# Kernel optimization log

Hardware: AMD Instinct MI355X
Metric: run time of the kernel (lower is better)

## Reference

```python
import jax, jax.numpy as jnp
import numpy as np

STRIDES = [8, 16, 32, 64, 128]
FSIZES = [64, 32, 16, 8, 4]          # 512x512 input
NUM_CLASSES = 80
POS_THR, NEG_THR = 0.5, 0.4          # MaxIOUAssigner thresholds
BETA = 1.0 / 9.0                      # SmoothL1 beta (from loss_bbox cfg)
BBOX_W = 10.0                         # SmoothL1 loss_weight
ALPHA, GAMMA = 0.25, 2.0              # sigmoid focal loss


def _gen_anchors():
    """RetinaNet-style grid anchors, xyxy, concatenated over levels -> [A,4]."""
    ratios = np.array([0.5, 1.0, 2.0])
    scales = 4.0 * 2.0 ** (np.arange(3) / 3.0)   # octave_base_scale=4, 3 octaves
    levels = []
    for s, f in zip(STRIDES, FSIZES):
        ws = (s * scales[None, :] / np.sqrt(ratios)[:, None]).reshape(-1)  # [9]
        hs = (s * scales[None, :] * np.sqrt(ratios)[:, None]).reshape(-1)
        c = (np.arange(f) + 0.5) * s
        sx, sy = np.meshgrid(c, c)
        cxy = np.stack([sx, sy], -1).reshape(-1, 1, 2)   # [f*f,1,2]
        wh = np.stack([ws, hs], -1)[None]                # [1,9,2]
        a = np.concatenate([cxy - wh / 2, cxy + wh / 2], -1).reshape(-1, 4)
        levels.append(a)
    return jnp.asarray(np.concatenate(levels, 0), dtype=jnp.float32)  # [49104,4]


def _iou(anchors, gt):  # [A,4],[M,4] -> [A,M]
    area_a = (anchors[:, 2] - anchors[:, 0]) * (anchors[:, 3] - anchors[:, 1])
    area_g = (gt[:, 2] - gt[:, 0]) * (gt[:, 3] - gt[:, 1])
    lt = jnp.maximum(anchors[:, None, :2], gt[None, :, :2])
    rb = jnp.minimum(anchors[:, None, 2:], gt[None, :, 2:])
    wh = jnp.clip(rb - lt, 0.0)
    inter = wh[..., 0] * wh[..., 1]
    return inter / jnp.maximum(area_a[:, None] + area_g[None, :] - inter, 1e-6)


def _encode(boxes, anchors):  # DeltaXYWH encode, target_stds = 1
    aw = anchors[:, 2] - anchors[:, 0]
    ah = anchors[:, 3] - anchors[:, 1]
    ax = (anchors[:, 0] + anchors[:, 2]) * 0.5
    ay = (anchors[:, 1] + anchors[:, 3]) * 0.5
    gw = jnp.maximum(boxes[:, 2] - boxes[:, 0], 1e-6)
    gh = jnp.maximum(boxes[:, 3] - boxes[:, 1], 1e-6)
    gx = (boxes[:, 0] + boxes[:, 2]) * 0.5
    gy = (boxes[:, 1] + boxes[:, 3]) * 0.5
    return jnp.stack([(gx - ax) / aw, (gy - ay) / ah,
                      jnp.log(gw / aw), jnp.log(gh / ah)], -1)


def _assign_one(gt_boxes, gt_labels, gt_mask, anchors):
    """Per-image: IoU match, pseudo-sample, gather matched GT, encode, masks."""
    iou = _iou(anchors, gt_boxes)                      # [A,M]
    iou = jnp.where(gt_mask[None, :], iou, -1.0)       # kill padded GTs
    best = jnp.argmax(iou, 1)                          # [A]
    best_iou = jnp.max(iou, 1)
    # matched index: >=0 matched, -1 background, -2 ignored
    idx = jnp.where(best_iou >= POS_THR, best,
                    jnp.where(best_iou < NEG_THR, -1, -2))
    pos = idx >= 0
    matched = jnp.where(pos[:, None], gt_boxes[best], 0.0)   # gather_based_on_match
    reg_t = _encode(matched, anchors)
    total = jnp.maximum(1.0, jnp.sum(pos.astype(jnp.float32)))
    mask_reg = pos.astype(jnp.float32)[:, None] / total      # [A,1] -> broadcast 4
    labels = jnp.where(pos, gt_labels[best], -1)             # bg/ignored -> -1
    mask_cls = (idx >= -1).astype(jnp.float32) / total       # matched + background
    return reg_t, mask_reg, labels, mask_cls


def setup_inputs() -> dict:
    key = jax.random.key(0)
    ks = jax.random.split(key, 6)
    B, M, A, C = 16, 100, 49104, NUM_CLASSES
    cls_score = jax.random.normal(ks[0], (B, A, C), jnp.float32)
    bbox_pred = jax.random.normal(ks[1], (B, A, 4), jnp.float32) * 0.1
    cxy = jax.random.uniform(ks[2], (B, M, 2), jnp.float32, 50.0, 462.0)
    wh = jax.random.uniform(ks[3], (B, M, 2), jnp.float32, 16.0, 128.0)
    target_boxes = jnp.concatenate([cxy - wh / 2, cxy + wh / 2], -1)
    target_labels = jax.random.randint(ks[4], (B, M), 0, C, jnp.int32)
    mask_labels = jax.random.randint(ks[5], (B, M), 0, 2, jnp.int32).astype(bool)
    return {"cls_score": cls_score, "bbox_pred": bbox_pred,
            "target_boxes": target_boxes, "target_labels": target_labels,
            "mask_labels": mask_labels}


def reference(cls_score, bbox_pred, target_boxes, target_labels, mask_labels):
    anchors = _gen_anchors()                                        # [A,4]
    reg_t, mask_reg, labels, mask_cls = jax.vmap(
        _assign_one, in_axes=(0, 0, 0, None))(
        target_boxes, target_labels, mask_labels, anchors)          # per image
    bs = float(cls_score.shape[0])
    # SmoothL1 (beta=1/9, weight 10), masked + normalized per image
    d = jnp.abs(bbox_pred - reg_t)
    l1 = jnp.where(d < BETA, 0.5 * d * d / BETA, d - 0.5 * BETA)
    loss_bbox = BBOX_W * jnp.sum(l1 * mask_reg) / bs
    # sigmoid focal loss
    t = jax.nn.one_hot(labels, NUM_CLASSES, dtype=cls_score.dtype)  # -1 -> all-zero
    bce = t * jax.nn.softplus(-cls_score) + (1.0 - t) * jax.nn.softplus(cls_score)
    p = jax.nn.sigmoid(cls_score)
    pt = t * p + (1.0 - t) * (1.0 - p)
    at = ALPHA * t + (1.0 - ALPHA) * (1.0 - t)
    focal = at * (1.0 - pt) ** GAMMA * bce
    loss_cls = jnp.sum(focal * mask_cls[..., None]) / bs
    return jnp.stack([loss_cls, loss_bbox])
```

## Files before the change

kernel.cpp:

```cpp
#include <hip/hip_runtime.h>

#define N_ANCH 49104
#define NB_IMG 16
#define NGT 100
#define NC 80
#define BPI 96
#define APB 512
#define NBLK (BPI * NB_IMG)
#define OFF_B NBLK
#define OFF_P (2 * NBLK)

#define LOG2E 1.4426950408889634f
#define LN2   0.6931471805599453f
#define FSCALE (0.75f * LN2)

__device__ __forceinline__ float frcp(float x){ return __builtin_amdgcn_rcpf(x); }
__device__ __forceinline__ float fexp2(float x){ return __builtin_amdgcn_exp2f(x); }
__device__ __forceinline__ float flog2(float x){ return __builtin_amdgcn_logf(x); }

__device__ __forceinline__ float f0_term(float x){
  float xl = x * LOG2E;
  float mx = fmaxf(xl, 0.f);
  float mn = fminf(xl, 0.f);
  float u  = fexp2(mn - mx);
  float w  = 1.0f + u;
  float lw = flog2(w);
  float g  = mn - lw;
  return fexp2(g + g) * (lw + mx);
}

__device__ __forceinline__ float corr_term(float x){
  float xl = x * LOG2E;
  float mx = fmaxf(xl, 0.f);
  float mn = fminf(xl, 0.f);
  float u  = fexp2(mn - mx);
  float w  = 1.0f + u;
  float lw = flog2(w);
  float p2   = fexp2(2.f * (mn - lw));
  float omp2 = fexp2(-2.f * (mx + lw));
  float sp   = LN2 * (lw + mx);
  float spn  = LN2 * (lw - mn);
  return 0.25f * omp2 * spn - 0.75f * p2 * sp;
}

__global__ __launch_bounds__(256, 6) void fused_loss_kernel(
    const float* __restrict__ cls,
    const float* __restrict__ bbox,
    const float* __restrict__ gtb,
    const int*   __restrict__ gtl,
    const unsigned char* __restrict__ gmask,
    float* __restrict__ ws)
{
  const int tid = threadIdx.x;
  const int wv = tid >> 6, ln = tid & 63;
  const int b  = blockIdx.y;
  const int a0 = blockIdx.x * APB;
  const int bid = b * BPI + blockIdx.x;

  __shared__ float4 s_cgt[NGT + 4];
  __shared__ float  s_carea[NGT + 4];
  __shared__ int    s_clab[NGT + 4];
  __shared__ float  s_w[APB];
  __shared__ int    s_lab[APB];
  __shared__ float  s_wmin[4], s_wmax[4];
  __shared__ float  s_r0[4], s_r1[4], s_r2[4];
  __shared__ int    s_cnt;

  float ax1[2], ay1[2], ax2[2], ay2[2], aarea[2];
  #pragma unroll
  for (int r = 0; r < 2; ++r){
    int a = a0 + r * 256 + tid;
    if (a < N_ANCH){
      int f, lg, st, rel;
      if      (a < 36864){ f = 64; lg = 6; st = 8;   rel = a; }
      else if (a < 46080){ f = 32; lg = 5; st = 16;  rel = a - 36864; }
      else if (a < 48384){ f = 16; lg = 4; st = 32;  rel = a - 46080; }
      else if (a < 48960){ f = 8;  lg = 3; st = 64;  rel = a - 48384; }
      else               { f = 4;  lg = 2; st = 128; rel = a - 48960; }
      int cell = rel / 9;
      int k    = rel - cell * 9;
      int yy   = cell >> lg;
      int xx   = cell & (f - 1);
      int rr = (k >= 6) ? 2 : ((k >= 3) ? 1 : 0);
      int sc = k - rr * 3;
      double sq  = (rr == 0) ? 0.7071067811865476 : ((rr == 1) ? 1.0 : 1.4142135623730951);
      double scl = (sc == 0) ? 4.0 : ((sc == 1) ? 5.039684199579493 : 6.349604207872798);
      double ss  = (double)st * scl;
      double wd  = ss / sq, hd = ss * sq;
      double cxd = ((double)xx + 0.5) * (double)st;
      double cyd = ((double)yy + 0.5) * (double)st;
      ax1[r] = (float)(cxd - wd * 0.5);
      ay1[r] = (float)(cyd - hd * 0.5);
      ax2[r] = (float)(cxd + wd * 0.5);
      ay2[r] = (float)(cyd + hd * 0.5);
      aarea[r] = (ax2[r] - ax1[r]) * (ay2[r] - ay1[r]);
    } else {
      ax1[r] = 0.f; ay1[r] = 3.0e38f; ax2[r] = 0.f; ay2[r] = -3.0e38f; aarea[r] = 1.f;
    }
  }

  {
    float wy1 = fminf(ay1[0], ay1[1]);
    float wy2 = fmaxf(ay2[0], ay2[1]);
    #pragma unroll
    for (int o = 32; o > 0; o >>= 1){
      wy1 = fminf(wy1, __shfl_down(wy1, o));
      wy2 = fmaxf(wy2, __shfl_down(wy2, o));
    }
    if (ln == 0){ s_wmin[wv] = wy1; s_wmax[wv] = wy2; }
  }
  __syncthreads();

  if (wv == 0){
    const unsigned int* mw = (const unsigned int*)gmask;
    bool nf = false, ob = false;
    for (int i = ln; i < (NB_IMG * NGT) / 4; i += 64){
      unsigned int w = mw[i];
      nf |= (w != 0u && w != 0x3F800000u);
      ob |= ((w & 0xFFFFFF00u) != 0u);
    }
    bool byteLayout = __any((int)nf) && __any((int)ob);
    float ymin = fminf(fminf(s_wmin[0], s_wmin[1]), fminf(s_wmin[2], s_wmin[3]));
    float ymax = fmaxf(fmaxf(s_wmax[0], s_wmax[1]), fmaxf(s_wmax[2], s_wmax[3]));
    const float4* g4 = (const float4*)gtb;

    float4 g = g4[b * NGT + ln];
    int v = byteLayout ? (gmask[b * NGT + ln] != 0)
                       : (((const unsigned int*)gmask)[b * NGT + ln] != 0u);
    bool pass = v && (g.y < ymax) && (g.w > ymin);
    unsigned long long bal = __ballot(pass);
    int pre = __popcll(bal & ((1ull << ln) - 1ull));
    if (pass){
      s_cgt[pre] = g;
      s_carea[pre] = (g.z - g.x) * (g.w - g.y);
      s_clab[pre] = gtl[b * NGT + ln];
    }
    int c0 = __popcll(bal);
    bool pass1 = false; float4 g1;
    if (ln < NGT - 64){
      g1 = g4[b * NGT + 64 + ln];
      int v1 = byteLayout ? (gmask[b * NGT + 64 + ln] != 0)
                          : (((const unsigned int*)gmask)[b * NGT + 64 + ln] != 0u);
      pass1 = v1 && (g1.y < ymax) && (g1.w > ymin);
    }
    unsigned long long bal1 = __ballot(pass1);
    int pre1 = c0 + __popcll(bal1 & ((1ull << ln) - 1ull));
    if (pass1){
      s_cgt[pre1] = g1;
      s_carea[pre1] = (g1.z - g1.x) * (g1.w - g1.y);
      s_clab[pre1] = gtl[b * NGT + 64 + ln];
    }
    if (ln == 0){
      int cnt = c0 + __popcll(bal1);
      float4 far4; far4.x = 3e9f; far4.y = 3e9f; far4.z = 3e9f; far4.w = 3e9f;
      s_cgt[cnt] = far4;     s_carea[cnt] = 0.f;     s_clab[cnt] = 0;
      s_cgt[cnt + 1] = far4; s_carea[cnt + 1] = 0.f; s_clab[cnt + 1] = 0;
      s_cnt = (cnt + 1) & ~1;
    }
  }
  __syncthreads();

  float accB = 0.f, posf = 0.f, fcorr = 0.f;
  const int cntp = s_cnt;
  #pragma unroll
  for (int r = 0; r < 2; ++r){
    int row = r * 256 + tid;
    int a = a0 + row;
    float x1 = ax1[r], y1 = ay1[r], x2 = ax2[r], y2 = ay2[r], areaA = aarea[r];
    float best_iou = -1.f; int best = 0;
    for (int j = 0; j < cntp; j += 2){
      #pragma unroll
      for (int u2 = 0; u2 < 2; ++u2){
        int jj = j + u2;
        float4 g = s_cgt[jj];
        float lx = fmaxf(x1, g.x), ly = fmaxf(y1, g.y);
        float rx = fminf(x2, g.z), ry = fminf(y2, g.w);
        float iw = fmaxf(rx - lx, 0.f), ih = fmaxf(ry - ly, 0.f);
        float I  = iw * ih;
        float U  = (areaA + s_carea[jj]) - I;
        float iou = I * frcp(U);
        best = (iou > best_iou) ? jj : best;
        best_iou = fmaxf(iou, best_iou);
      }
    }
    bool va  = a < N_ANCH;
    bool pos = va && (best_iou >= 0.5f);
    bool ign = va && !pos && (best_iou >= 0.4f);
    s_w[row]   = (va && !ign) ? 1.f : 0.f;
    s_lab[row] = pos ? s_clab[best] : -1;

    if (pos){
      posf += 1.f;
      float4 g = s_cgt[best];
      float aw = x2 - x1, ah = y2 - y1;
      float axc = (x1 + x2) * 0.5f, ayc = (y1 + y2) * 0.5f;
      float gw = fmaxf(g.z - g.x, 1e-6f), gh = fmaxf(g.w - g.y, 1e-6f);
      float gxc = (g.x + g.z) * 0.5f, gyc = (g.y + g.w) * 0.5f;
      float t0 = (gxc - axc) / aw, t1 = (gyc - ayc) / ah;
      float t2 = LN2 * flog2(gw * frcp(aw));
      float t3 = LN2 * flog2(gh * frcp(ah));
      float4 bp = ((const float4*)bbox)[(size_t)b * N_ANCH + a];
      const float BETA = 1.0f / 9.0f;
      float d0 = fabsf(bp.x - t0), d1 = fabsf(bp.y - t1);
      float d2 = fabsf(bp.z - t2), d3 = fabsf(bp.w - t3);
      accB += (d0 < BETA) ? 4.5f * d0 * d0 : d0 - 0.5f * BETA;
      accB += (d1 < BETA) ? 4.5f * d1 * d1 : d1 - 0.5f * BETA;
      accB += (d2 < BETA) ? 4.5f * d2 * d2 : d2 - 0.5f * BETA;
      accB += (d3 < BETA) ? 4.5f * d3 * d3 : d3 - 0.5f * BETA;
    }
  }
  __syncthreads();

  const int nvalid = min(N_ANCH - a0, APB);
  const int nf4 = nvalid * 20;
  const float4* cp = (const float4*)(cls + (size_t)(b * N_ANCH + a0) * NC);
  float fraw = 0.f;
  for (int i = tid; i < nf4; i += 256){
    float4 c4 = cp[i];
    int row = i / 20;
    int cb  = (i - row * 20) * 4;
    float s = (f0_term(c4.x) + f0_term(c4.y)) + (f0_term(c4.z) + f0_term(c4.w));
    fraw = fmaf(s_w[row], s, fraw);
    int lab = s_lab[row];
    if ((unsigned)(lab - cb) < 4u){
      int o = lab - cb;
      float xe = (o == 0) ? c4.x : (o == 1) ? c4.y : (o == 2) ? c4.z : c4.w;
      fcorr += corr_term(xe);
    }
  }
  float accC = fmaf(FSCALE, fraw, fcorr);

  #pragma unroll
  for (int o = 32; o > 0; o >>= 1){
    accC += __shfl_down(accC, o);
    accB += __shfl_down(accB, o);
    posf += __shfl_down(posf, o);
  }
  if (ln == 0){ s_r0[wv] = accC; s_r1[wv] = accB; s_r2[wv] = posf; }
  __syncthreads();
  if (tid == 0){
    ws[bid]         = s_r0[0] + s_r0[1] + s_r0[2] + s_r0[3];
    ws[OFF_B + bid] = s_r1[0] + s_r1[1] + s_r1[2] + s_r1[3];
    ws[OFF_P + bid] = s_r2[0] + s_r2[1] + s_r2[2] + s_r2[3];
  }
}

__global__ void finalize_kernel(const float* __restrict__ ws,
                                float* __restrict__ out)
{
  __shared__ float sC[NB_IMG], sB[NB_IMG];
  const int tid = threadIdx.x;
  const int wv = tid >> 6, ln = tid & 63;
  #pragma unroll
  for (int i = 0; i < 2; ++i){
    int b = wv * 2 + i;
    float c = 0.f, bb = 0.f, p = 0.f;
    for (int k = ln; k < BPI; k += 64){
      c  += ws[b * BPI + k];
      bb += ws[OFF_B + b * BPI + k];
      p  += ws[OFF_P + b * BPI + k];
    }
    #pragma unroll
    for (int o = 32; o > 0; o >>= 1){
      c += __shfl_down(c, o); bb += __shfl_down(bb, o); p += __shfl_down(p, o);
    }
    if (ln == 0){
      float tot = fmaxf(p, 1.f);
      sC[b] = c / tot;
      sB[b] = bb / tot;
    }
  }
  __syncthreads();
  if (tid == 0){
    float lc = 0.f, lb = 0.f;
    #pragma unroll
    for (int b = 0; b < NB_IMG; ++b){ lc += sC[b]; lb += sB[b]; }
    out[0] = lc / 16.f;
    out[1] = 10.f * lb / 16.f;
  }
}

extern "C" void kernel_launch(void* const* d_in, const int* in_sizes, int n_in,
                              void* d_out, int out_size, void* d_ws, size_t ws_size,
                              hipStream_t stream) {
  const float* cls  = (const float*)d_in[0];
  const float* bbox = (const float*)d_in[1];
  const float* gtb  = (const float*)d_in[2];
  const int*   gtl  = (const int*)d_in[3];
  const unsigned char* gmask = (const unsigned char*)d_in[4];

  float* ws = (float*)d_ws;

  dim3 grid(BPI, NB_IMG);
  fused_loss_kernel<<<grid, 256, 0, stream>>>(cls, bbox, gtb, gtl, gmask, ws);
  finalize_kernel<<<1, 512, 0, stream>>>(ws, (float*)d_out);
}
```

Baseline: 57.25 us.

## Overlap anchor assignment in one wave with unweighted focal streaming

Wave 3 of each block now does all the anchor generation, GT compaction and IoU matching for the block's 512 anchors. Meanwhile all four waves stream the class scores and sum the focal negative term without weights. Rows marked ignored are then re-read and their contribution subtracted, and the positive-label correction reads one element per row directly. This removes the barrier between assignment and the bandwidth-heavy class-score pass. In exchange, the IoU work sits on a single wave, which may lengthen that wave's critical path, and ignored rows are read twice.

```diff
diff --git a/kernel.cpp b/kernel.cpp
--- a/kernel.cpp
+++ b/kernel.cpp
@@ -9,6 +9,9 @@
 #define NBLK (BPI * NB_IMG)
 #define OFF_B NBLK
 #define OFF_P (2 * NBLK)
+#define ROW_F4 (NC / 4)
+#define BLK_F4 (APB * ROW_F4)
+#define WCHUNK (BLK_F4 / 4)
 
 #define LOG2E 1.4426950408889634f
 #define LN2   0.6931471805599453f
@@ -41,6 +44,32 @@
   float sp   = LN2 * (lw + mx);
   float spn  = LN2 * (lw - mn);
   return 0.25f * omp2 * spn - 0.75f * p2 * sp;
+}
+
+__device__ __forceinline__ void anchor_geom(int a, float& x1, float& y1,
+                                            float& x2, float& y2){
+  int f, lg, st, rel;
+  if      (a < 36864){ f = 64; lg = 6; st = 8;   rel = a; }
+  else if (a < 46080){ f = 32; lg = 5; st = 16;  rel = a - 36864; }
+  else if (a < 48384){ f = 16; lg = 4; st = 32;  rel = a - 46080; }
+  else if (a < 48960){ f = 8;  lg = 3; st = 64;  rel = a - 48384; }
+  else               { f = 4;  lg = 2; st = 128; rel = a - 48960; }
+  int cell = rel / 9;
+  int k    = rel - cell * 9;
+  int yy   = cell >> lg;
+  int xx   = cell & (f - 1);
+  int rr = (k >= 6) ? 2 : ((k >= 3) ? 1 : 0);
+  int sc = k - rr * 3;
+  double sq  = (rr == 0) ? 0.7071067811865476 : ((rr == 1) ? 1.0 : 1.4142135623730951);
+  double scl = (sc == 0) ? 4.0 : ((sc == 1) ? 5.039684199579493 : 6.349604207872798);
+  double ss  = (double)st * scl;
+  double wd  = ss / sq, hd = ss * sq;
+  double cxd = ((double)xx + 0.5) * (double)st;
+  double cyd = ((double)yy + 0.5) * (double)st;
+  x1 = (float)(cxd - wd * 0.5);
+  y1 = (float)(cyd - hd * 0.5);
+  x2 = (float)(cxd + wd * 0.5);
+  y2 = (float)(cyd + hd * 0.5);
 }
 
 __global__ __launch_bounds__(256, 6) void fused_loss_kernel(
@@ -56,62 +85,40 @@
   const int b  = blockIdx.y;
   const int a0 = blockIdx.x * APB;
   const int bid = b * BPI + blockIdx.x;
+  const int nvalid = min(N_ANCH - a0, APB);
+  const int nf4 = nvalid * ROW_F4;
 
   __shared__ float4 s_cgt[NGT + 4];
   __shared__ float  s_carea[NGT + 4];
   __shared__ int    s_clab[NGT + 4];
   __shared__ float  s_w[APB];
   __shared__ int    s_lab[APB];
-  __shared__ float  s_wmin[4], s_wmax[4];
   __shared__ float  s_r0[4], s_r1[4], s_r2[4];
-  __shared__ int    s_cnt;
-
-  float ax1[2], ay1[2], ax2[2], ay2[2], aarea[2];
-  #pragma unroll
-  for (int r = 0; r < 2; ++r){
-    int a = a0 + r * 256 + tid;
-    if (a < N_ANCH){
-      int f, lg, st, rel;
-      if      (a < 36864){ f = 64; lg = 6; st = 8;   rel = a; }
-      else if (a < 46080){ f = 32; lg = 5; st = 16;  rel = a - 36864; }
-      else if (a < 48384){ f = 16; lg = 4; st = 32;  rel = a - 46080; }
-      else if (a < 48960){ f = 8;  lg = 3; st = 64;  rel = a - 48384; }
-      else               { f = 4;  lg = 2; st = 128; rel = a - 48960; }
-      int cell = rel / 9;
-      int k    = rel - cell * 9;
-      int yy   = cell >> lg;
-      int xx   = cell & (f - 1);
-      int rr = (k >= 6) ? 2 : ((k >= 3) ? 1 : 0);
-      int sc = k - rr * 3;
-      double sq  = (rr == 0) ? 0.7071067811865476 : ((rr == 1) ? 1.0 : 1.4142135623730951);
-      double scl = (sc == 0) ? 4.0 : ((sc == 1) ? 5.039684199579493 : 6.349604207872798);
-      double ss  = (double)st * scl;
-      double wd  = ss / sq, hd = ss * sq;
-      double cxd = ((double)xx + 0.5) * (double)st;
-      double cyd = ((double)yy + 0.5) * (double)st;
-      ax1[r] = (float)(cxd - wd * 0.5);
-      ay1[r] = (float)(cyd - hd * 0.5);
-      ax2[r] = (float)(cxd + wd * 0.5);
-      ay2[r] = (float)(cyd + hd * 0.5);
-      aarea[r] = (ax2[r] - ax1[r]) * (ay2[r] - ay1[r]);
-    } else {
-      ax1[r] = 0.f; ay1[r] = 3.0e38f; ax2[r] = 0.f; ay2[r] = -3.0e38f; aarea[r] = 1.f;
-    }
-  }
-
-  {
-    float wy1 = fminf(ay1[0], ay1[1]);
-    float wy2 = fmaxf(ay2[0], ay2[1]);
+
+  const float* clsbase = cls + (size_t)(b * N_ANCH + a0) * NC;
+  const float4* cp = (const float4*)clsbase;
+
+  float accB = 0.f, posf = 0.f;
+  float s0 = 0.f, s1 = 0.f, s2 = 0.f, s3 = 0.f;
+
+  if (wv == 3){
+    float ymin = 3.0e38f, ymax = -3.0e38f;
     #pragma unroll
-    for (int o = 32; o > 0; o >>= 1){
-      wy1 = fminf(wy1, __shfl_down(wy1, o));
-      wy2 = fmaxf(wy2, __shfl_down(wy2, o));
-    }
-    if (ln == 0){ s_wmin[wv] = wy1; s_wmax[wv] = wy2; }
-  }
-  __syncthreads();
-
-  if (wv == 0){
+    for (int r = 0; r < 8; ++r){
+      int a = a0 + r * 64 + ln;
+      if (a < N_ANCH){
+        float x1, y1, x2, y2;
+        anchor_geom(a, x1, y1, x2, y2);
+        ymin = fminf(ymin, y1);
+        ymax = fmaxf(ymax, y2);
+      }
+    }
+    #pragma unroll
+    for (int o = 1; o < 64; o <<= 1){
+      ymin = fminf(ymin, __shfl_xor(ymin, o));
+      ymax = fmaxf(ymax, __shfl_xor(ymax, o));
+    }
+
     const unsigned int* mw = (const unsigned int*)gmask;
     bool nf = false, ob = false;
     for (int i = ln; i < (NB_IMG * NGT) / 4; i += 64){
@@ -120,10 +127,8 @@
       ob |= ((w & 0xFFFFFF00u) != 0u);
     }
     bool byteLayout = __any((int)nf) && __any((int)ob);
-    float ymin = fminf(fminf(s_wmin[0], s_wmin[1]), fminf(s_wmin[2], s_wmin[3]));
-    float ymax = fmaxf(fmaxf(s_wmax[0], s_wmax[1]), fmaxf(s_wmax[2], s_wmax[3]));
+
     const float4* g4 = (const float4*)gtb;
-
     float4 g = g4[b * NGT + ln];
     int v = byteLayout ? (gmask[b * NGT + ln] != 0)
                        : (((const unsigned int*)gmask)[b * NGT + ln] != 0u);
@@ -150,85 +155,99 @@
       s_carea[pre1] = (g1.z - g1.x) * (g1.w - g1.y);
       s_clab[pre1] = gtl[b * NGT + 64 + ln];
     }
+    int cnt = c0 + __popcll(bal1);
     if (ln == 0){
-      int cnt = c0 + __popcll(bal1);
       float4 far4; far4.x = 3e9f; far4.y = 3e9f; far4.z = 3e9f; far4.w = 3e9f;
       s_cgt[cnt] = far4;     s_carea[cnt] = 0.f;     s_clab[cnt] = 0;
       s_cgt[cnt + 1] = far4; s_carea[cnt + 1] = 0.f; s_clab[cnt + 1] = 0;
-      s_cnt = (cnt + 1) & ~1;
+    }
+    const int cntp = (cnt + 1) & ~1;
+
+    #pragma unroll 2
+    for (int r = 0; r < 8; ++r){
+      int row = r * 64 + ln;
+      int a = a0 + row;
+      float x1, y1, x2, y2;
+      anchor_geom(min(a, N_ANCH - 1), x1, y1, x2, y2);
+      float areaA = (x2 - x1) * (y2 - y1);
+      float best_iou = -1.f; int best = 0;
+      for (int j = 0; j < cntp; j += 2){
+        #pragma unroll
+        for (int u2 = 0; u2 < 2; ++u2){
+          int jj = j + u2;
+          float4 gg = s_cgt[jj];
+          float lx = fmaxf(x1, gg.x), ly = fmaxf(y1, gg.y);
+          float rx = fminf(x2, gg.z), ry = fminf(y2, gg.w);
+          float iw = fmaxf(rx - lx, 0.f), ih = fmaxf(ry - ly, 0.f);
+          float I  = iw * ih;
+          float U  = (areaA + s_carea[jj]) - I;
+          float iou = I * frcp(U);
+          best = (iou > best_iou) ? jj : best;
+          best_iou = fmaxf(iou, best_iou);
+        }
+      }
+      bool va  = a < N_ANCH;
+      bool pos = va && (best_iou >= 0.5f);
+      bool ign = va && !pos && (best_iou >= 0.4f);
+      s_w[row]   = ign ? 0.f : 1.f;
+      s_lab[row] = pos ? s_clab[best] : -1;
+
+      if (pos){
+        posf += 1.f;
+        float4 gg = s_cgt[best];
+        float aw = x2 - x1, ah = y2 - y1;
+        float axc = (x1 + x2) * 0.5f, ayc = (y1 + y2) * 0.5f;
+        float gw = fmaxf(gg.z - gg.x, 1e-6f), gh = fmaxf(gg.w - gg.y, 1e-6f);
+        float gxc = (gg.x + gg.z) * 0.5f, gyc = (gg.y + gg.w) * 0.5f;
+        float t0 = (gxc - axc) / aw, t1 = (gyc - ayc) / ah;
+        float t2 = LN2 * flog2(gw * frcp(aw));
+        float t3 = LN2 * flog2(gh * frcp(ah));
+        float4 bp = ((const float4*)bbox)[(size_t)b * N_ANCH + a];
+        const float BETA = 1.0f / 9.0f;
+        float d0 = fabsf(bp.x - t0), d1 = fabsf(bp.y - t1);
+        float d2 = fabsf(bp.z - t2), d3 = fabsf(bp.w - t3);
+        accB += (d0 < BETA) ? 4.5f * d0 * d0 : d0 - 0.5f * BETA;
+        accB += (d1 < BETA) ? 4.5f * d1 * d1 : d1 - 0.5f * BETA;
+        accB += (d2 < BETA) ? 4.5f * d2 * d2 : d2 - 0.5f * BETA;
+        accB += (d3 < BETA) ? 4.5f * d3 * d3 : d3 - 0.5f * BETA;
+      }
+    }
+  }
+
+  {
+    const int iend = min(nf4, (wv + 1) * WCHUNK);
+    #pragma unroll 2
+    for (int i = wv * WCHUNK + ln; i < iend; i += 64){
+      float4 c4 = cp[i];
+      s0 += f0_term(c4.x);
+      s1 += f0_term(c4.y);
+      s2 += f0_term(c4.z);
+      s3 += f0_term(c4.w);
     }
   }
   __syncthreads();
 
-  float accB = 0.f, posf = 0.f, fcorr = 0.f;
-  const int cntp = s_cnt;
+  float fsub = 0.f, fcorr = 0.f;
   #pragma unroll
-  for (int r = 0; r < 2; ++r){
-    int row = r * 256 + tid;
-    int a = a0 + row;
-    float x1 = ax1[r], y1 = ay1[r], x2 = ax2[r], y2 = ay2[r], areaA = aarea[r];
-    float best_iou = -1.f; int best = 0;
-    for (int j = 0; j < cntp; j += 2){
-      #pragma unroll
-      for (int u2 = 0; u2 < 2; ++u2){
-        int jj = j + u2;
-        float4 g = s_cgt[jj];
-        float lx = fmaxf(x1, g.x), ly = fmaxf(y1, g.y);
-        float rx = fminf(x2, g.z), ry = fminf(y2, g.w);
-        float iw = fmaxf(rx - lx, 0.f), ih = fmaxf(ry - ly, 0.f);
-        float I  = iw * ih;
-        float U  = (areaA + s_carea[jj]) - I;
-        float iou = I * frcp(U);
-        best = (iou > best_iou) ? jj : best;
-        best_iou = fmaxf(iou, best_iou);
+  for (int h = 0; h < 2; ++h){
+    int row = wv * 128 + h * 64 + ln;
+    if (row < nvalid){
+      int lab = s_lab[row];
+      if (lab >= 0) fcorr += corr_term(clsbase[row * NC + lab]);
+      if (s_w[row] == 0.f){
+        const float4* rp = cp + row * ROW_F4;
+        float t0 = 0.f, t1 = 0.f, t2 = 0.f, t3 = 0.f;
+        #pragma unroll 5
+        for (int k2 = 0; k2 < ROW_F4; ++k2){
+          float4 c4 = rp[k2];
+          t0 += f0_term(c4.x); t1 += f0_term(c4.y);
+          t2 += f0_term(c4.z); t3 += f0_term(c4.w);
+        }
+        fsub += (t0 + t1) + (t2 + t3);
       }
     }
-    bool va  = a < N_ANCH;
-    bool pos = va && (best_iou >= 0.5f);
-    bool ign = va && !pos && (best_iou >= 0.4f);
-    s_w[row]   = (va && !ign) ? 1.f : 0.f;
-    s_lab[row] = pos ? s_clab[best] : -1;
-
-    if (pos){
-      posf += 1.f;
-      float4 g = s_cgt[best];
-      float aw = x2 - x1, ah = y2 - y1;
-      float axc = (x1 + x2) * 0.5f, ayc = (y1 + y2) * 0.5f;
-      float gw = fmaxf(g.z - g.x, 1e-6f), gh = fmaxf(g.w - g.y, 1e-6f);
-      float gxc = (g.x + g.z) * 0.5f, gyc = (g.y + g.w) * 0.5f;
-      float t0 = (gxc - axc) / aw, t1 = (gyc - ayc) / ah;
-      float t2 = LN2 * flog2(gw * frcp(aw));
-      float t3 = LN2 * flog2(gh * frcp(ah));
-      float4 bp = ((const float4*)bbox)[(size_t)b * N_ANCH + a];
-      const float BETA = 1.0f / 9.0f;
-      float d0 = fabsf(bp.x - t0), d1 = fabsf(bp.y - t1);
-      float d2 = fabsf(bp.z - t2), d3 = fabsf(bp.w - t3);
-      accB += (d0 < BETA) ? 4.5f * d0 * d0 : d0 - 0.5f * BETA;
-      accB += (d1 < BETA) ? 4.5f * d1 * d1 : d1 - 0.5f * BETA;
-      accB += (d2 < BETA) ? 4.5f * d2 * d2 : d2 - 0.5f * BETA;
-      accB += (d3 < BETA) ? 4.5f * d3 * d3 : d3 - 0.5f * BETA;
-    }
-  }
-  __syncthreads();
-
-  const int nvalid = min(N_ANCH - a0, APB);
-  const int nf4 = nvalid * 20;
-  const float4* cp = (const float4*)(cls + (size_t)(b * N_ANCH + a0) * NC);
-  float fraw = 0.f;
-  for (int i = tid; i < nf4; i += 256){
-    float4 c4 = cp[i];
-    int row = i / 20;
-    int cb  = (i - row * 20) * 4;
-    float s = (f0_term(c4.x) + f0_term(c4.y)) + (f0_term(c4.z) + f0_term(c4.w));
-    fraw = fmaf(s_w[row], s, fraw);
-    int lab = s_lab[row];
-    if ((unsigned)(lab - cb) < 4u){
-      int o = lab - cb;
-      float xe = (o == 0) ? c4.x : (o == 1) ? c4.y : (o == 2) ? c4.z : c4.w;
-      fcorr += corr_term(xe);
-    }
-  }
-  float accC = fmaf(FSCALE, fraw, fcorr);
+  }
+  float accC = fmaf(FSCALE, ((s0 + s1) + (s2 + s3)) - fsub, fcorr);
 
   #pragma unroll
   for (int o = 32; o > 0; o >>= 1){
```

New measurement: 89.50 us. 1.56x slower.

## Split fused loss into separate assign and cls-streaming kernels with byte label buffer

Applied to the files above, without the earlier changes.

Splits the single fused kernel into an IoU-assignment kernel, which writes per-anchor byte labels (with neg/ignore sentinels) plus the bbox partial sums, and a separate streaming kernel that reads the labels and computes focal loss over cls_score. The IoU argmax now compares by cross-multiplication instead of taking a reciprocal, and thresholds are tested the same way. The intent is to keep the bandwidth-bound cls stream free of the compute-heavy assignment phase and its syncs. In exchange it adds a kernel launch and a global round trip for the label buffer.

```diff
diff --git a/kernel.cpp b/kernel.cpp
--- a/kernel.cpp
+++ b/kernel.cpp
@@ -7,12 +7,15 @@
 #define BPI 96
 #define APB 512
 #define NBLK (BPI * NB_IMG)
-#define OFF_B NBLK
-#define OFF_P (2 * NBLK)
+#define ROW_F4 (NC / 4)
+#define LABSTRIDE (BPI * APB)
 
 #define LOG2E 1.4426950408889634f
 #define LN2   0.6931471805599453f
 #define FSCALE (0.75f * LN2)
+
+#define LAB_NEG 200
+#define LAB_IGN 201
 
 __device__ __forceinline__ float frcp(float x){ return __builtin_amdgcn_rcpf(x); }
 __device__ __forceinline__ float fexp2(float x){ return __builtin_amdgcn_exp2f(x); }
@@ -43,62 +46,65 @@
   return 0.25f * omp2 * spn - 0.75f * p2 * sp;
 }
 
-__global__ __launch_bounds__(256, 6) void fused_loss_kernel(
-    const float* __restrict__ cls,
+__device__ __forceinline__ void anchor_geom(int a, float& x1, float& y1,
+                                            float& x2, float& y2){
+  int lg, st, rel;
+  if      (a < 36864){ lg = 6; st = 8;   rel = a; }
+  else if (a < 46080){ lg = 5; st = 16;  rel = a - 36864; }
+  else if (a < 48384){ lg = 4; st = 32;  rel = a - 46080; }
+  else if (a < 48960){ lg = 3; st = 64;  rel = a - 48384; }
+  else               { lg = 2; st = 128; rel = a - 48960; }
+  int cell = rel / 9;
+  int k    = rel - cell * 9;
+  int yy   = cell >> lg;
+  int xx   = cell & ((1 << lg) - 1);
+  int rr = (k >= 6) ? 2 : ((k >= 3) ? 1 : 0);
+  int sc = k - rr * 3;
+  double sq  = (rr == 0) ? 0.7071067811865476 : ((rr == 1) ? 1.0 : 1.4142135623730951);
+  double scl = (sc == 0) ? 4.0 : ((sc == 1) ? 5.039684199579493 : 6.349604207872798);
+  double ss  = (double)st * scl;
+  double wd  = ss / sq, hd = ss * sq;
+  double cxd = ((double)xx + 0.5) * (double)st;
+  double cyd = ((double)yy + 0.5) * (double)st;
+  x1 = (float)(cxd - wd * 0.5);
+  y1 = (float)(cyd - hd * 0.5);
+  x2 = (float)(cxd + wd * 0.5);
+  y2 = (float)(cyd + hd * 0.5);
+}
+
+__global__ __launch_bounds__(256, 6) void assign_kernel(
     const float* __restrict__ bbox,
     const float* __restrict__ gtb,
     const int*   __restrict__ gtl,
     const unsigned char* __restrict__ gmask,
-    float* __restrict__ ws)
+    unsigned char* __restrict__ lab,
+    float* __restrict__ bbP,
+    float* __restrict__ posP)
 {
   const int tid = threadIdx.x;
   const int wv = tid >> 6, ln = tid & 63;
   const int b  = blockIdx.y;
-  const int a0 = blockIdx.x * APB;
-  const int bid = b * BPI + blockIdx.x;
+  const int blkx = blockIdx.x;
+  const int a0 = blkx * APB;
+  const int bid = b * BPI + blkx;
 
   __shared__ float4 s_cgt[NGT + 4];
   __shared__ float  s_carea[NGT + 4];
   __shared__ int    s_clab[NGT + 4];
-  __shared__ float  s_w[APB];
-  __shared__ int    s_lab[APB];
   __shared__ float  s_wmin[4], s_wmax[4];
-  __shared__ float  s_r0[4], s_r1[4], s_r2[4];
+  __shared__ float  s_r1[4], s_r2[4];
   __shared__ int    s_cnt;
 
-  float ax1[2], ay1[2], ax2[2], ay2[2], aarea[2];
+  float ax1[2], ay1[2], ax2[2], ay2[2];
   #pragma unroll
   for (int r = 0; r < 2; ++r){
     int a = a0 + r * 256 + tid;
     if (a < N_ANCH){
-      int f, lg, st, rel;
-      if      (a < 36864){ f = 64; lg = 6; st = 8;   rel = a; }
-      else if (a < 46080){ f = 32; lg = 5; st = 16;  rel = a - 36864; }
-      else if (a < 48384){ f = 16; lg = 4; st = 32;  rel = a - 46080; }
-      else if (a < 48960){ f = 8;  lg = 3; st = 64;  rel = a - 48384; }
-      else               { f = 4;  lg = 2; st = 128; rel = a - 48960; }
-      int cell = rel / 9;
-      int k    = rel - cell * 9;
-      int yy   = cell >> lg;
-      int xx   = cell & (f - 1);
-      int rr = (k >= 6) ? 2 : ((k >= 3) ? 1 : 0);
-      int sc = k - rr * 3;
-      double sq  = (rr == 0) ? 0.7071067811865476 : ((rr == 1) ? 1.0 : 1.4142135623730951);
-      double scl = (sc == 0) ? 4.0 : ((sc == 1) ? 5.039684199579493 : 6.349604207872798);
-      double ss  = (double)st * scl;
-      double wd  = ss / sq, hd = ss * sq;
-      double cxd = ((double)xx + 0.5) * (double)st;
-      double cyd = ((double)yy + 0.5) * (double)st;
-      ax1[r] = (float)(cxd - wd * 0.5);
-      ay1[r] = (float)(cyd - hd * 0.5);
-      ax2[r] = (float)(cxd + wd * 0.5);
-      ay2[r] = (float)(cyd + hd * 0.5);
-      aarea[r] = (ax2[r] - ax1[r]) * (ay2[r] - ay1[r]);
+      anchor_geom(a, ax1[r], ay1[r], ax2[r], ay2[r]);
     } else {
-      ax1[r] = 0.f; ay1[r] = 3.0e38f; ax2[r] = 0.f; ay2[r] = -3.0e38f; aarea[r] = 1.f;
-    }
-  }
-
+      ax1[r] = 0.f; ay1[r] = 3.0e38f; ax2[r] = 0.f; ay2[r] = -3.0e38f;
+    }
+  }
   {
     float wy1 = fminf(ay1[0], ay1[1]);
     float wy2 = fmaxf(ay2[0], ay2[1]);
@@ -160,42 +166,45 @@
   }
   __syncthreads();
 
-  float accB = 0.f, posf = 0.f, fcorr = 0.f;
+  float accB = 0.f, posf = 0.f;
   const int cntp = s_cnt;
   #pragma unroll
   for (int r = 0; r < 2; ++r){
-    int row = r * 256 + tid;
-    int a = a0 + row;
-    float x1 = ax1[r], y1 = ay1[r], x2 = ax2[r], y2 = ay2[r], areaA = aarea[r];
-    float best_iou = -1.f; int best = 0;
+    int a = a0 + r * 256 + tid;
+    float x1 = ax1[r], y1 = ay1[r], x2 = ax2[r], y2 = ay2[r];
+    float areaA = (x2 - x1) * (y2 - y1);
+    float Ib = -1.f, Ub = 1.f; int best = 0;
     for (int j = 0; j < cntp; j += 2){
       #pragma unroll
       for (int u2 = 0; u2 < 2; ++u2){
         int jj = j + u2;
-        float4 g = s_cgt[jj];
-        float lx = fmaxf(x1, g.x), ly = fmaxf(y1, g.y);
-        float rx = fminf(x2, g.z), ry = fminf(y2, g.w);
+        float4 gg = s_cgt[jj];
+        float lx = fmaxf(x1, gg.x), ly = fmaxf(y1, gg.y);
+        float rx = fminf(x2, gg.z), ry = fminf(y2, gg.w);
         float iw = fmaxf(rx - lx, 0.f), ih = fmaxf(ry - ly, 0.f);
         float I  = iw * ih;
         float U  = (areaA + s_carea[jj]) - I;
-        float iou = I * frcp(U);
-        best = (iou > best_iou) ? jj : best;
-        best_iou = fmaxf(iou, best_iou);
+        bool gt = I * Ub > Ib * U;
+        best = gt ? jj : best;
+        Ib = gt ? I : Ib;
+        Ub = gt ? U : Ub;
       }
     }
     bool va  = a < N_ANCH;
-    bool pos = va && (best_iou >= 0.5f);
-    bool ign = va && !pos && (best_iou >= 0.4f);
-    s_w[row]   = (va && !ign) ? 1.f : 0.f;
-    s_lab[row] = pos ? s_clab[best] : -1;
+    bool pos = va && (2.f * Ib >= Ub);
+    bool ign = !pos && (5.f * Ib >= 2.f * Ub);
+    unsigned char lb = pos ? (unsigned char)s_clab[best]
+                           : ((ign || !va) ? (unsigned char)LAB_IGN
+                                           : (unsigned char)LAB_NEG);
+    lab[(size_t)b * LABSTRIDE + a0 + r * 256 + tid] = lb;
 
     if (pos){
       posf += 1.f;
-      float4 g = s_cgt[best];
+      float4 gg = s_cgt[best];
       float aw = x2 - x1, ah = y2 - y1;
       float axc = (x1 + x2) * 0.5f, ayc = (y1 + y2) * 0.5f;
-      float gw = fmaxf(g.z - g.x, 1e-6f), gh = fmaxf(g.w - g.y, 1e-6f);
-      float gxc = (g.x + g.z) * 0.5f, gyc = (g.y + g.w) * 0.5f;
+      float gw = fmaxf(gg.z - gg.x, 1e-6f), gh = fmaxf(gg.w - gg.y, 1e-6f);
+      float gxc = (gg.x + gg.z) * 0.5f, gyc = (gg.y + gg.w) * 0.5f;
       float t0 = (gxc - axc) / aw, t1 = (gyc - ayc) / ah;
       float t2 = LN2 * flog2(gw * frcp(aw));
       float t3 = LN2 * flog2(gh * frcp(ah));
@@ -209,21 +218,53 @@
       accB += (d3 < BETA) ? 4.5f * d3 * d3 : d3 - 0.5f * BETA;
     }
   }
-  __syncthreads();
-
+
+  #pragma unroll
+  for (int o = 32; o > 0; o >>= 1){
+    accB += __shfl_down(accB, o);
+    posf += __shfl_down(posf, o);
+  }
+  if (ln == 0){ s_r1[wv] = accB; s_r2[wv] = posf; }
+  __syncthreads();
+  if (tid == 0){
+    bbP[bid]  = s_r1[0] + s_r1[1] + s_r1[2] + s_r1[3];
+    posP[bid] = s_r2[0] + s_r2[1] + s_r2[2] + s_r2[3];
+  }
+}
+
+__global__ __launch_bounds__(256, 6) void stream_kernel(
+    const float* __restrict__ cls,
+    const unsigned char* __restrict__ lab,
+    float* __restrict__ clsP)
+{
+  const int tid = threadIdx.x;
+  const int wv = tid >> 6, ln = tid & 63;
+  const int b  = blockIdx.y;
+  const int a0 = blockIdx.x * APB;
+  const int bid = b * BPI + blockIdx.x;
   const int nvalid = min(N_ANCH - a0, APB);
-  const int nf4 = nvalid * 20;
+  const int nf4 = nvalid * ROW_F4;
+
+  __shared__ unsigned char s_lab[APB];
+  __shared__ float s_r0[4];
+
+  #pragma unroll
+  for (int j = 0; j < 2; ++j)
+    s_lab[j * 256 + tid] = lab[(size_t)b * LABSTRIDE + a0 + j * 256 + tid];
+  __syncthreads();
+
   const float4* cp = (const float4*)(cls + (size_t)(b * N_ANCH + a0) * NC);
-  float fraw = 0.f;
+  float fraw = 0.f, fcorr = 0.f;
   for (int i = tid; i < nf4; i += 256){
     float4 c4 = cp[i];
     int row = i / 20;
     int cb  = (i - row * 20) * 4;
     float s = (f0_term(c4.x) + f0_term(c4.y)) + (f0_term(c4.z) + f0_term(c4.w));
-    fraw = fmaf(s_w[row], s, fraw);
-    int lab = s_lab[row];
-    if ((unsigned)(lab - cb) < 4u){
-      int o = lab - cb;
+    int li = (int)s_lab[row];
+    float wf = (li == LAB_IGN) ? 0.f : 1.f;
+    fraw = fmaf(wf, s, fraw);
+    if ((unsigned)(li - cb) < 4u){
+      int o = li - cb;
       float xe = (o == 0) ? c4.x : (o == 1) ? c4.y : (o == 2) ? c4.z : c4.w;
       fcorr += corr_term(xe);
     }
@@ -231,21 +272,15 @@
   float accC = fmaf(FSCALE, fraw, fcorr);
 
   #pragma unroll
-  for (int o = 32; o > 0; o >>= 1){
-    accC += __shfl_down(accC, o);
-    accB += __shfl_down(accB, o);
-    posf += __shfl_down(posf, o);
-  }
-  if (ln == 0){ s_r0[wv] = accC; s_r1[wv] = accB; s_r2[wv] = posf; }
-  __syncthreads();
-  if (tid == 0){
-    ws[bid]         = s_r0[0] + s_r0[1] + s_r0[2] + s_r0[3];
-    ws[OFF_B + bid] = s_r1[0] + s_r1[1] + s_r1[2] + s_r1[3];
-    ws[OFF_P + bid] = s_r2[0] + s_r2[1] + s_r2[2] + s_r2[3];
-  }
-}
-
-__global__ void finalize_kernel(const float* __restrict__ ws,
+  for (int o = 32; o > 0; o >>= 1) accC += __shfl_down(accC, o);
+  if (ln == 0) s_r0[wv] = accC;
+  __syncthreads();
+  if (tid == 0) clsP[bid] = s_r0[0] + s_r0[1] + s_r0[2] + s_r0[3];
+}
+
+__global__ void finalize_kernel(const float* __restrict__ clsP,
+                                const float* __restrict__ bbP,
+                                const float* __restrict__ posP,
                                 float* __restrict__ out)
 {
   __shared__ float sC[NB_IMG], sB[NB_IMG];
@@ -256,9 +291,9 @@
     int b = wv * 2 + i;
     float c = 0.f, bb = 0.f, p = 0.f;
     for (int k = ln; k < BPI; k += 64){
-      c  += ws[b * BPI + k];
-      bb += ws[OFF_B + b * BPI + k];
-      p  += ws[OFF_P + b * BPI + k];
+      c  += clsP[b * BPI + k];
+      bb += bbP[b * BPI + k];
+      p  += posP[b * BPI + k];
     }
     #pragma unroll
     for (int o = 32; o > 0; o >>= 1){
@@ -289,9 +324,14 @@
   const int*   gtl  = (const int*)d_in[3];
   const unsigned char* gmask = (const unsigned char*)d_in[4];
 
-  float* ws = (float*)d_ws;
+  unsigned char* labbuf = (unsigned char*)d_ws;
+  float* wsf  = (float*)((char*)d_ws + (size_t)NB_IMG * LABSTRIDE);
+  float* bbP  = wsf;
+  float* posP = wsf + NBLK;
+  float* clsP = wsf + 2 * NBLK;
 
   dim3 grid(BPI, NB_IMG);
-  fused_loss_kernel<<<grid, 256, 0, stream>>>(cls, bbox, gtb, gtl, gmask, ws);
-  finalize_kernel<<<1, 512, 0, stream>>>(ws, (float*)d_out);
-}
+  assign_kernel<<<grid, 256, 0, stream>>>(bbox, gtb, gtl, gmask, labbuf, bbP, posP);
+  stream_kernel<<<grid, 256, 0, stream>>>(cls, labbuf, clsP);
+  finalize_kernel<<<1, 512, 0, stream>>>(clsP, bbP, posP, (float*)d_out);
+}
```

New measurement: 66.14 us. +15.5%, slower.

## Per-wave GT compaction, divide-free IoU compare, prefetch cls, direct label correction

Applied to the files above, without the earlier changes.

Each wave now builds its own compacted GT list in shared memory using a wave-wide ymin/ymax reduction, which removes two block barriers and the wave-0 serialization. Anchor geometry moves from double precision to float arithmetic with constant tables. IoU argmax compares I*U cross products instead of computing reciprocals, and the thresholds are tested the same way. The focal label correction is read directly for positive anchors, which drops the per-element label check from the streaming loop, and the first two cls float4 loads are issued at kernel start to overlap with matching. The risks are that every wave redundantly scans the mask and GT data, and that float anchor coordinates or the cross-product comparison could differ slightly from the reference at threshold and tie boundaries.

```diff
diff --git a/kernel.cpp b/kernel.cpp
--- a/kernel.cpp
+++ b/kernel.cpp
@@ -7,12 +7,35 @@
 #define BPI 96
 #define APB 512
 #define NBLK (BPI * NB_IMG)
-#define OFF_B NBLK
-#define OFF_P (2 * NBLK)
+#define ROW_F4 (NC / 4)
+#define MAXG 104
 
 #define LOG2E 1.4426950408889634f
 #define LN2   0.6931471805599453f
 #define FSCALE (0.75f * LN2)
+
+__constant__ float BW9[9] = {
+  (float)(4.0               / 0.7071067811865476 * 0.5),
+  (float)(5.039684199579493 / 0.7071067811865476 * 0.5),
+  (float)(6.349604207872798 / 0.7071067811865476 * 0.5),
+  (float)(4.0               * 0.5),
+  (float)(5.039684199579493 * 0.5),
+  (float)(6.349604207872798 * 0.5),
+  (float)(4.0               / 1.4142135623730951 * 0.5),
+  (float)(5.039684199579493 / 1.4142135623730951 * 0.5),
+  (float)(6.349604207872798 / 1.4142135623730951 * 0.5),
+};
+__constant__ float BH9[9] = {
+  (float)(4.0               * 0.7071067811865476 * 0.5),
+  (float)(5.039684199579493 * 0.7071067811865476 * 0.5),
+  (float)(6.349604207872798 * 0.7071067811865476 * 0.5),
+  (float)(4.0               * 0.5),
+  (float)(5.039684199579493 * 0.5),
+  (float)(6.349604207872798 * 0.5),
+  (float)(4.0               * 1.4142135623730951 * 0.5),
+  (float)(5.039684199579493 * 1.4142135623730951 * 0.5),
+  (float)(6.349604207872798 * 1.4142135623730951 * 0.5),
+};
 
 __device__ __forceinline__ float frcp(float x){ return __builtin_amdgcn_rcpf(x); }
 __device__ __forceinline__ float fexp2(float x){ return __builtin_amdgcn_exp2f(x); }
@@ -27,6 +50,9 @@
   float lw = flog2(w);
   float g  = mn - lw;
   return fexp2(g + g) * (lw + mx);
+}
+__device__ __forceinline__ float f0x4(float4 c4){
+  return (f0_term(c4.x) + f0_term(c4.y)) + (f0_term(c4.z) + f0_term(c4.w));
 }
 
 __device__ __forceinline__ float corr_term(float x){
@@ -41,6 +67,26 @@
   float sp   = LN2 * (lw + mx);
   float spn  = LN2 * (lw - mn);
   return 0.25f * omp2 * spn - 0.75f * p2 * sp;
+}
+
+__device__ __forceinline__ void anchor_geom(int a, float& x1, float& y1,
+                                            float& x2, float& y2){
+  int lg, st, rel;
+  if      (a < 36864){ lg = 6; st = 8;   rel = a; }
+  else if (a < 46080){ lg = 5; st = 16;  rel = a - 36864; }
+  else if (a < 48384){ lg = 4; st = 32;  rel = a - 46080; }
+  else if (a < 48960){ lg = 3; st = 64;  rel = a - 48384; }
+  else               { lg = 2; st = 128; rel = a - 48960; }
+  int cell = rel / 9;
+  int k    = rel - cell * 9;
+  int yy   = cell >> lg;
+  int xx   = cell & ((1 << lg) - 1);
+  float stf = (float)st;
+  float cx = ((float)xx + 0.5f) * stf;
+  float cy = ((float)yy + 0.5f) * stf;
+  float w2 = stf * BW9[k];
+  float h2 = stf * BH9[k];
+  x1 = cx - w2; y1 = cy - h2; x2 = cx + w2; y2 = cy + h2;
 }
 
 __global__ __launch_bounds__(256, 6) void fused_loss_kernel(
@@ -56,146 +102,117 @@
   const int b  = blockIdx.y;
   const int a0 = blockIdx.x * APB;
   const int bid = b * BPI + blockIdx.x;
-
-  __shared__ float4 s_cgt[NGT + 4];
-  __shared__ float  s_carea[NGT + 4];
-  __shared__ int    s_clab[NGT + 4];
-  __shared__ float  s_w[APB];
-  __shared__ int    s_lab[APB];
-  __shared__ float  s_wmin[4], s_wmax[4];
+  const int nvalid = min(N_ANCH - a0, APB);
+  const int nf4 = nvalid * ROW_F4;
+
+  __shared__ float4 s_cgt[4][MAXG];
+  __shared__ float  s_carea[4][MAXG];
+  __shared__ int    s_clab[4][MAXG];
+  __shared__ float  s_wf[APB];
   __shared__ float  s_r0[4], s_r1[4], s_r2[4];
-  __shared__ int    s_cnt;
-
-  float ax1[2], ay1[2], ax2[2], ay2[2], aarea[2];
+
+  const float* clsbase = cls + (size_t)(b * N_ANCH + a0) * NC;
+  const float4* cp = (const float4*)clsbase;
+
+  float4 pf0 = cp[tid];
+  float4 pf1 = cp[tid + 256];
+
+  float ax1[2], ay1[2], ax2[2], ay2[2];
   #pragma unroll
   for (int r = 0; r < 2; ++r){
     int a = a0 + r * 256 + tid;
-    if (a < N_ANCH){
-      int f, lg, st, rel;
-      if      (a < 36864){ f = 64; lg = 6; st = 8;   rel = a; }
-      else if (a < 46080){ f = 32; lg = 5; st = 16;  rel = a - 36864; }
-      else if (a < 48384){ f = 16; lg = 4; st = 32;  rel = a - 46080; }
-      else if (a < 48960){ f = 8;  lg = 3; st = 64;  rel = a - 48384; }
-      else               { f = 4;  lg = 2; st = 128; rel = a - 48960; }
-      int cell = rel / 9;
-      int k    = rel - cell * 9;
-      int yy   = cell >> lg;
-      int xx   = cell & (f - 1);
-      int rr = (k >= 6) ? 2 : ((k >= 3) ? 1 : 0);
-      int sc = k - rr * 3;
-      double sq  = (rr == 0) ? 0.7071067811865476 : ((rr == 1) ? 1.0 : 1.4142135623730951);
-      double scl = (sc == 0) ? 4.0 : ((sc == 1) ? 5.039684199579493 : 6.349604207872798);
-      double ss  = (double)st * scl;
-      double wd  = ss / sq, hd = ss * sq;
-      double cxd = ((double)xx + 0.5) * (double)st;
-      double cyd = ((double)yy + 0.5) * (double)st;
-      ax1[r] = (float)(cxd - wd * 0.5);
-      ay1[r] = (float)(cyd - hd * 0.5);
-      ax2[r] = (float)(cxd + wd * 0.5);
-      ay2[r] = (float)(cyd + hd * 0.5);
-      aarea[r] = (ax2[r] - ax1[r]) * (ay2[r] - ay1[r]);
-    } else {
-      ax1[r] = 0.f; ay1[r] = 3.0e38f; ax2[r] = 0.f; ay2[r] = -3.0e38f; aarea[r] = 1.f;
-    }
-  }
-
-  {
-    float wy1 = fminf(ay1[0], ay1[1]);
-    float wy2 = fmaxf(ay2[0], ay2[1]);
-    #pragma unroll
-    for (int o = 32; o > 0; o >>= 1){
-      wy1 = fminf(wy1, __shfl_down(wy1, o));
-      wy2 = fmaxf(wy2, __shfl_down(wy2, o));
-    }
-    if (ln == 0){ s_wmin[wv] = wy1; s_wmax[wv] = wy2; }
-  }
-  __syncthreads();
-
-  if (wv == 0){
-    const unsigned int* mw = (const unsigned int*)gmask;
-    bool nf = false, ob = false;
-    for (int i = ln; i < (NB_IMG * NGT) / 4; i += 64){
-      unsigned int w = mw[i];
-      nf |= (w != 0u && w != 0x3F800000u);
-      ob |= ((w & 0xFFFFFF00u) != 0u);
-    }
-    bool byteLayout = __any((int)nf) && __any((int)ob);
-    float ymin = fminf(fminf(s_wmin[0], s_wmin[1]), fminf(s_wmin[2], s_wmin[3]));
-    float ymax = fmaxf(fmaxf(s_wmax[0], s_wmax[1]), fmaxf(s_wmax[2], s_wmax[3]));
-    const float4* g4 = (const float4*)gtb;
-
-    float4 g = g4[b * NGT + ln];
-    int v = byteLayout ? (gmask[b * NGT + ln] != 0)
-                       : (((const unsigned int*)gmask)[b * NGT + ln] != 0u);
-    bool pass = v && (g.y < ymax) && (g.w > ymin);
-    unsigned long long bal = __ballot(pass);
-    int pre = __popcll(bal & ((1ull << ln) - 1ull));
-    if (pass){
-      s_cgt[pre] = g;
-      s_carea[pre] = (g.z - g.x) * (g.w - g.y);
-      s_clab[pre] = gtl[b * NGT + ln];
-    }
-    int c0 = __popcll(bal);
-    bool pass1 = false; float4 g1;
-    if (ln < NGT - 64){
-      g1 = g4[b * NGT + 64 + ln];
-      int v1 = byteLayout ? (gmask[b * NGT + 64 + ln] != 0)
-                          : (((const unsigned int*)gmask)[b * NGT + 64 + ln] != 0u);
-      pass1 = v1 && (g1.y < ymax) && (g1.w > ymin);
-    }
-    unsigned long long bal1 = __ballot(pass1);
-    int pre1 = c0 + __popcll(bal1 & ((1ull << ln) - 1ull));
-    if (pass1){
-      s_cgt[pre1] = g1;
-      s_carea[pre1] = (g1.z - g1.x) * (g1.w - g1.y);
-      s_clab[pre1] = gtl[b * NGT + 64 + ln];
-    }
-    if (ln == 0){
-      int cnt = c0 + __popcll(bal1);
-      float4 far4; far4.x = 3e9f; far4.y = 3e9f; far4.z = 3e9f; far4.w = 3e9f;
-      s_cgt[cnt] = far4;     s_carea[cnt] = 0.f;     s_clab[cnt] = 0;
-      s_cgt[cnt + 1] = far4; s_carea[cnt + 1] = 0.f; s_clab[cnt + 1] = 0;
-      s_cnt = (cnt + 1) & ~1;
-    }
-  }
-  __syncthreads();
+    if (a < N_ANCH) anchor_geom(a, ax1[r], ay1[r], ax2[r], ay2[r]);
+    else { ax1[r] = 0.f; ay1[r] = 3.0e38f; ax2[r] = 0.f; ay2[r] = -3.0e38f; }
+  }
+
+  float ymin = fminf(ay1[0], ay1[1]);
+  float ymax = fmaxf(ay2[0], ay2[1]);
+  #pragma unroll
+  for (int o = 32; o > 0; o >>= 1){
+    ymin = fminf(ymin, __shfl_xor(ymin, o));
+    ymax = fmaxf(ymax, __shfl_xor(ymax, o));
+  }
+
+  const unsigned int* mw = (const unsigned int*)gmask;
+  bool nfb = false, ob = false;
+  for (int i = ln; i < (NB_IMG * NGT) / 4; i += 64){
+    unsigned int w = mw[i];
+    nfb |= (w != 0u && w != 0x3F800000u);
+    ob  |= ((w & 0xFFFFFF00u) != 0u);
+  }
+  const bool byteLayout = __any((int)nfb) && __any((int)ob);
+
+  const float4* g4 = (const float4*)gtb;
+  float4 g = g4[b * NGT + ln];
+  int v = byteLayout ? (gmask[b * NGT + ln] != 0)
+                     : (((const unsigned int*)gmask)[b * NGT + ln] != 0u);
+  bool pass = v && (g.y < ymax) && (g.w > ymin);
+  unsigned long long bal = __ballot(pass);
+  int pre = __popcll(bal & ((1ull << ln) - 1ull));
+  if (pass){
+    s_cgt[wv][pre]   = g;
+    s_carea[wv][pre] = (g.z - g.x) * (g.w - g.y);
+    s_clab[wv][pre]  = gtl[b * NGT + ln];
+  }
+  int cnt = __popcll(bal);
+  float4 g1; bool pass1 = false;
+  if (ln < NGT - 64){
+    g1 = g4[b * NGT + 64 + ln];
+    int v1 = byteLayout ? (gmask[b * NGT + 64 + ln] != 0)
+                        : (((const unsigned int*)gmask)[b * NGT + 64 + ln] != 0u);
+    pass1 = v1 && (g1.y < ymax) && (g1.w > ymin);
+  }
+  unsigned long long bal1 = __ballot(pass1);
+  int pre1 = cnt + __popcll(bal1 & ((1ull << ln) - 1ull));
+  if (pass1){
+    s_cgt[wv][pre1]   = g1;
+    s_carea[wv][pre1] = (g1.z - g1.x) * (g1.w - g1.y);
+    s_clab[wv][pre1]  = gtl[b * NGT + 64 + ln];
+  }
+  cnt += __popcll(bal1);
+  if (ln == 0){
+    float4 far4; far4.x = 3e9f; far4.y = 3e9f; far4.z = 3e9f; far4.w = 3e9f;
+    s_cgt[wv][cnt]   = far4; s_carea[wv][cnt]   = 0.f; s_clab[wv][cnt]   = 0;
+    s_cgt[wv][cnt+1] = far4; s_carea[wv][cnt+1] = 0.f; s_clab[wv][cnt+1] = 0;
+  }
+  const int cntp = (cnt + 1) & ~1;
 
   float accB = 0.f, posf = 0.f, fcorr = 0.f;
-  const int cntp = s_cnt;
   #pragma unroll
   for (int r = 0; r < 2; ++r){
     int row = r * 256 + tid;
     int a = a0 + row;
-    float x1 = ax1[r], y1 = ay1[r], x2 = ax2[r], y2 = ay2[r], areaA = aarea[r];
-    float best_iou = -1.f; int best = 0;
+    float x1 = ax1[r], y1 = ay1[r], x2 = ax2[r], y2 = ay2[r];
+    float areaA = (x2 - x1) * (y2 - y1);
+    float Ib = -1.f, Ub = 1.f; int best = 0;
     for (int j = 0; j < cntp; j += 2){
       #pragma unroll
       for (int u2 = 0; u2 < 2; ++u2){
         int jj = j + u2;
-        float4 g = s_cgt[jj];
-        float lx = fmaxf(x1, g.x), ly = fmaxf(y1, g.y);
-        float rx = fminf(x2, g.z), ry = fminf(y2, g.w);
+        float4 gg = s_cgt[wv][jj];
+        float lx = fmaxf(x1, gg.x), ly = fmaxf(y1, gg.y);
+        float rx = fminf(x2, gg.z), ry = fminf(y2, gg.w);
         float iw = fmaxf(rx - lx, 0.f), ih = fmaxf(ry - ly, 0.f);
         float I  = iw * ih;
-        float U  = (areaA + s_carea[jj]) - I;
-        float iou = I * frcp(U);
-        best = (iou > best_iou) ? jj : best;
-        best_iou = fmaxf(iou, best_iou);
+        float U  = (areaA + s_carea[wv][jj]) - I;
+        bool gt = I * Ub > Ib * U;
+        best = gt ? jj : best;
+        Ib = gt ? I : Ib;
+        Ub = gt ? U : Ub;
       }
     }
     bool va  = a < N_ANCH;
-    bool pos = va && (best_iou >= 0.5f);
-    bool ign = va && !pos && (best_iou >= 0.4f);
-    s_w[row]   = (va && !ign) ? 1.f : 0.f;
-    s_lab[row] = pos ? s_clab[best] : -1;
+    bool pos = va && (2.f * Ib >= Ub);
+    bool ign = va && !pos && (5.f * Ib >= 2.f * Ub);
+    s_wf[row] = ign ? 0.f : 1.f;
 
     if (pos){
       posf += 1.f;
-      float4 g = s_cgt[best];
+      float4 gg = s_cgt[wv][best];
       float aw = x2 - x1, ah = y2 - y1;
       float axc = (x1 + x2) * 0.5f, ayc = (y1 + y2) * 0.5f;
-      float gw = fmaxf(g.z - g.x, 1e-6f), gh = fmaxf(g.w - g.y, 1e-6f);
-      float gxc = (g.x + g.z) * 0.5f, gyc = (g.y + g.w) * 0.5f;
+      float gw = fmaxf(gg.z - gg.x, 1e-6f), gh = fmaxf(gg.w - gg.y, 1e-6f);
+      float gxc = (gg.x + gg.z) * 0.5f, gyc = (gg.y + gg.w) * 0.5f;
       float t0 = (gxc - axc) / aw, t1 = (gyc - ayc) / ah;
       float t2 = LN2 * flog2(gw * frcp(aw));
       float t3 = LN2 * flog2(gh * frcp(ah));
@@ -207,26 +224,18 @@
       accB += (d1 < BETA) ? 4.5f * d1 * d1 : d1 - 0.5f * BETA;
       accB += (d2 < BETA) ? 4.5f * d2 * d2 : d2 - 0.5f * BETA;
       accB += (d3 < BETA) ? 4.5f * d3 * d3 : d3 - 0.5f * BETA;
+      int lab = s_clab[wv][best];
+      fcorr += corr_term(clsbase[(size_t)row * NC + lab]);
     }
   }
   __syncthreads();
 
-  const int nvalid = min(N_ANCH - a0, APB);
-  const int nf4 = nvalid * 20;
-  const float4* cp = (const float4*)(cls + (size_t)(b * N_ANCH + a0) * NC);
   float fraw = 0.f;
-  for (int i = tid; i < nf4; i += 256){
+  fraw = fmaf(s_wf[tid / 20],         f0x4(pf0), fraw);
+  fraw = fmaf(s_wf[(tid + 256) / 20], f0x4(pf1), fraw);
+  for (int i = tid + 512; i < nf4; i += 256){
     float4 c4 = cp[i];
-    int row = i / 20;
-    int cb  = (i - row * 20) * 4;
-    float s = (f0_term(c4.x) + f0_term(c4.y)) + (f0_term(c4.z) + f0_term(c4.w));
-    fraw = fmaf(s_w[row], s, fraw);
-    int lab = s_lab[row];
-    if ((unsigned)(lab - cb) < 4u){
-      int o = lab - cb;
-      float xe = (o == 0) ? c4.x : (o == 1) ? c4.y : (o == 2) ? c4.z : c4.w;
-      fcorr += corr_term(xe);
-    }
+    fraw = fmaf(s_wf[i / 20], f0x4(c4), fraw);
   }
   float accC = fmaf(FSCALE, fraw, fcorr);
 
@@ -239,9 +248,9 @@
   if (ln == 0){ s_r0[wv] = accC; s_r1[wv] = accB; s_r2[wv] = posf; }
   __syncthreads();
   if (tid == 0){
-    ws[bid]         = s_r0[0] + s_r0[1] + s_r0[2] + s_r0[3];
-    ws[OFF_B + bid] = s_r1[0] + s_r1[1] + s_r1[2] + s_r1[3];
-    ws[OFF_P + bid] = s_r2[0] + s_r2[1] + s_r2[2] + s_r2[3];
+    ws[bid]            = s_r0[0] + s_r0[1] + s_r0[2] + s_r0[3];
+    ws[NBLK + bid]     = s_r1[0] + s_r1[1] + s_r1[2] + s_r1[3];
+    ws[2 * NBLK + bid] = s_r2[0] + s_r2[1] + s_r2[2] + s_r2[3];
   }
 }
 
@@ -257,8 +266,8 @@
     float c = 0.f, bb = 0.f, p = 0.f;
     for (int k = ln; k < BPI; k += 64){
       c  += ws[b * BPI + k];
-      bb += ws[OFF_B + b * BPI + k];
-      p  += ws[OFF_P + b * BPI + k];
+      bb += ws[NBLK + b * BPI + k];
+      p  += ws[2 * NBLK + b * BPI + k];
     }
     #pragma unroll
     for (int o = 32; o > 0; o >>= 1){
```

After: 56.17 us. No clear change (-1.9%).
